# Kernel optimization log

Hardware: AMD Instinct MI355X
Metric: run time of the kernel (lower is better)

The kernel has to match this reference:

```python
import jax, jax.numpy as jnp
import numpy as np

EPS = 1e-8  # torch cosine_similarity norm clamp

def _cos(a, b, axis=-1):
    na = jnp.maximum(jnp.linalg.norm(a, axis=axis), EPS)
    nb = jnp.maximum(jnp.linalg.norm(b, axis=axis), EPS)
    return jnp.sum(a * b, axis=axis) / (na * nb)

def setup_inputs() -> dict:
    key = jax.random.key(0)
    ks = jax.random.split(key, 9)
    B, L, D, S = 8, 8192, 512, 131072
    scale = 0.02
    x = jax.random.normal(ks[0], (B, L, D), jnp.float32)
    context_W = jax.random.normal(ks[1], (D, D), jnp.float32) * scale
    context_b = jnp.zeros((D,), jnp.float32)
    pred_W1 = jax.random.normal(ks[2], (D, D), jnp.float32) * scale
    pred_b1 = jnp.zeros((D,), jnp.float32)
    pred_W2 = jax.random.normal(ks[3], (D, D), jnp.float32) * scale
    pred_b2 = jnp.zeros((D,), jnp.float32)
    raw_embeddings = jax.random.normal(ks[4], (S, D), jnp.float32)
    u = jax.random.uniform(ks[5], (S,), jnp.float32)
    surprise_level = jnp.where(u > 0.5, u, 0.0)  # ~half the slots active
    return {"x": x, "context_W": context_W, "context_b": context_b,
            "pred_W1": pred_W1, "pred_b1": pred_b1,
            "pred_W2": pred_W2, "pred_b2": pred_b2,
            "raw_embeddings": raw_embeddings, "surprise_level": surprise_level}

def reference(x, context_W, context_b, pred_W1, pred_b1, pred_W2, pred_b2,
              raw_embeddings, surprise_level):
    # context = pad(x[:, :-1], left-shift by one along seq), i.e. causal previous token
    context = jnp.pad(x[:, :-1, :], ((0, 0), (1, 0), (0, 0)))
    # predictor MLP on projected context (torch Linear: y = x @ W.T + b)
    ctx = context @ context_W.T + context_b
    h = jax.nn.gelu(ctx @ pred_W1.T + pred_b1, approximate=False)
    prediction = h @ pred_W2.T + pred_b2  # [B, L, D]
    mse = jnp.mean((x - prediction) ** 2, axis=-1)
    prediction_surprise = jnp.sqrt(mse)  # [B, L]

    # memory-contrastive surprise: cosine sim of pooled x vs active stored embeddings
    active = surprise_level > 0  # [S]
    x_pooled = jnp.mean(x, axis=1)  # [B, D]
    sim = _cos(x_pooled[:, None, :], raw_embeddings[None, :, :])  # [B, S]
    sim = jnp.where(active[None, :], sim, -jnp.inf)
    max_sim = jnp.max(sim, axis=-1)           # [B]
    best_idx = jnp.argmax(sim, axis=-1)       # [B]
    best_stored = raw_embeddings[best_idx]    # [B, D] argmax-based gather
    divergence = 1.0 - _cos(x, best_stored[:, None, :])  # [B, L]
    pattern_match = (max_sim[:, None] > 0.3).astype(x.dtype)
    contrastive = pattern_match * divergence

    surprise = jnp.maximum(prediction_surprise, contrastive * 2.0)  # [B, L]
    return surprise
```

## Files before the change

### kernel.cpp

```cpp
#include <hip/hip_runtime.h>
#include <math.h>

#define OFF_SIMKEY   0
#define OFF_POOLED   1024
#define ZEROED_BYTES 17408
#define OFF_MAXSIM   17408
#define OFF_NORME    17664
#define OFF_EBEST    17920
#define OFF_BPRIME   34304
#define OFF_WP       36864
#define OFF_W2B      561152

typedef __attribute__((ext_vector_type(8))) short bf16x8;
typedef __attribute__((ext_vector_type(4))) float f32x4;

__device__ inline unsigned short f2bf(float f) {
    unsigned int u = __float_as_uint(f);
    unsigned int r = (u + 0x7FFFu + ((u >> 16) & 1u)) >> 16;
    return (unsigned short)r;
}

__device__ inline void load_lds_16(const void* g, void* l) {
    __builtin_amdgcn_global_load_lds((const __attribute__((address_space(1))) void*)g,
                                     (__attribute__((address_space(3))) void*)l, 16, 0, 0);
}

__global__ void __launch_bounds__(256) k_pre(const float* __restrict__ W1, const float* __restrict__ Wc,
                      const float* __restrict__ b1, const float* __restrict__ bc,
                      unsigned short* __restrict__ Wp, float* __restrict__ bprime) {
    __shared__ float w1row[512];
    __shared__ float wsum[4];
    int t = threadIdx.x;
    int n = blockIdx.x >> 1, half = blockIdx.x & 1;
    if (t < 128) ((float4*)w1row)[t] = ((const float4*)(W1 + (size_t)n * 512))[t];
    __syncthreads();
    int k = half * 256 + t;
    float acc = 0.f;
#pragma unroll 8
    for (int j = 0; j < 512; ++j) acc += w1row[j] * Wc[(size_t)j * 512 + k];
    Wp[(size_t)n * 512 + k] = f2bf(acc);
    if (half == 0) {
        float p = w1row[t] * bc[t] + w1row[t + 256] * bc[t + 256];
#pragma unroll
        for (int m = 32; m >= 1; m >>= 1) p += __shfl_xor(p, m);
        if ((t & 63) == 0) wsum[t >> 6] = p;
        __syncthreads();
        if (t == 0) bprime[n] = b1[n] + wsum[0] + wsum[1] + wsum[2] + wsum[3];
    }
}

__global__ void __launch_bounds__(256) k_cast(const float* __restrict__ W2, unsigned short* __restrict__ W2b) {
    int i = blockIdx.x * 1024 + threadIdx.x * 4;
    float4 v = *(const float4*)(W2 + i);
    ushort4 o;
    o.x = f2bf(v.x); o.y = f2bf(v.y); o.z = f2bf(v.z); o.w = f2bf(v.w);
    *(ushort4*)(W2b + i) = o;
}

__global__ void __launch_bounds__(512) k_pool(const float* __restrict__ x, float* __restrict__ pooled) {
    __shared__ float4 pb[4][128];
    int t = threadIdx.x;
    int q = t & 127;
    int rg = t >> 7;
    int b = blockIdx.y;
    int l0 = blockIdx.x * 128;
    const float4* p = (const float4*)(x + ((size_t)b * 8192 + l0 + rg) * 512) + q;
    float4 s = make_float4(0.f, 0.f, 0.f, 0.f);
#pragma unroll 8
    for (int i = 0; i < 32; ++i) {
        float4 v = p[(size_t)i * 512];
        s.x += v.x; s.y += v.y; s.z += v.z; s.w += v.w;
    }
    pb[rg][q] = s;
    __syncthreads();
    if (rg == 0) {
        float4 a = pb[0][q], b1_ = pb[1][q], c = pb[2][q], d = pb[3][q];
        atomicAdd(&pooled[b * 512 + q * 4 + 0], a.x + b1_.x + c.x + d.x);
        atomicAdd(&pooled[b * 512 + q * 4 + 1], a.y + b1_.y + c.y + d.y);
        atomicAdd(&pooled[b * 512 + q * 4 + 2], a.z + b1_.z + c.z + d.z);
        atomicAdd(&pooled[b * 512 + q * 4 + 3], a.w + b1_.w + c.w + d.w);
    }
}

__global__ void __launch_bounds__(256) k_sim(const float* __restrict__ E, const float* __restrict__ sl,
                     const float* __restrict__ pooledws, unsigned long long* __restrict__ simkey) {
    __shared__ float ps[4096];
    __shared__ unsigned long long wkey[4][8];
    int t = threadIdx.x, lane = t & 63, w = t >> 6;
#pragma unroll
    for (int c = 0; c < 16; ++c) ps[t + c * 256] = pooledws[t + c * 256] * (1.0f / 8192.0f);
    __syncthreads();
    float pr[8][8];
#pragma unroll
    for (int b = 0; b < 8; ++b) {
        float4 v0 = *(const float4*)&ps[b * 512 + lane * 8];
        float4 v1 = *(const float4*)&ps[b * 512 + lane * 8 + 4];
        pr[b][0] = v0.x; pr[b][1] = v0.y; pr[b][2] = v0.z; pr[b][3] = v0.w;
        pr[b][4] = v1.x; pr[b][5] = v1.y; pr[b][6] = v1.z; pr[b][7] = v1.w;
    }
    float npinv[8];
#pragma unroll
    for (int b = 0; b < 8; ++b) {
        float s = 0.f;
#pragma unroll
        for (int j = 0; j < 8; ++j) s += pr[b][j] * pr[b][j];
#pragma unroll
        for (int m = 32; m >= 1; m >>= 1) s += __shfl_xor(s, m);
        npinv[b] = 1.0f / fmaxf(sqrtf(s), 1e-8f);
    }
    unsigned long long best[8];
#pragma unroll
    for (int b = 0; b < 8; ++b) best[b] = 0ull;
    int sbase = blockIdx.x * 64 + w * 16;
    float mysl = (lane < 16) ? sl[sbase + lane] : 0.f;
    unsigned long long mask = __ballot(mysl > 0.0f);
    for (int it = 0; it < 16; ++it) {
        if (!((mask >> it) & 1ull)) continue;
        int s = sbase + it;
        const float4* ep = (const float4*)(E + (size_t)s * 512);
        float4 e0 = ep[lane * 2], e1 = ep[lane * 2 + 1];
        float nrm = e0.x * e0.x + e0.y * e0.y + e0.z * e0.z + e0.w * e0.w
                  + e1.x * e1.x + e1.y * e1.y + e1.z * e1.z + e1.w * e1.w;
        float dt[8];
#pragma unroll
        for (int b = 0; b < 8; ++b)
            dt[b] = e0.x * pr[b][0] + e0.y * pr[b][1] + e0.z * pr[b][2] + e0.w * pr[b][3]
                  + e1.x * pr[b][4] + e1.y * pr[b][5] + e1.z * pr[b][6] + e1.w * pr[b][7];
#pragma unroll
        for (int m = 32; m >= 1; m >>= 1) {
            nrm += __shfl_xor(nrm, m);
#pragma unroll
            for (int b = 0; b < 8; ++b) dt[b] += __shfl_xor(dt[b], m);
        }
        float neinv = 1.0f / fmaxf(sqrtf(nrm), 1e-8f);
#pragma unroll
        for (int b = 0; b < 8; ++b) {
            float sim = dt[b] * npinv[b] * neinv;
            unsigned int u = __float_as_uint(sim);
            unsigned int k32 = (u & 0x80000000u) ? ~u : (u | 0x80000000u);
            unsigned long long key = ((unsigned long long)k32 << 32) | (unsigned int)(~(unsigned int)s);
            if (key > best[b]) best[b] = key;
        }
    }
    if (lane == 0) {
#pragma unroll
        for (int b = 0; b < 8; ++b) wkey[w][b] = best[b];
    }
    __syncthreads();
    if (t < 8) {
        unsigned long long k = wkey[0][t];
#pragma unroll
        for (int w2 = 1; w2 < 4; ++w2) if (wkey[w2][t] > k) k = wkey[w2][t];
        if (k) atomicMax(&simkey[t], k);
    }
}

__global__ void __launch_bounds__(64) k_b2(const float* __restrict__ E, const unsigned long long* __restrict__ simkey,
                    float* __restrict__ max_sim, float* __restrict__ norm_e, float* __restrict__ ebest) {
    int b = blockIdx.x, lane = threadIdx.x;
    unsigned long long key = simkey[b];
    float ms; unsigned int idx;
    if (key == 0ull) { ms = -1e30f; idx = 0u; }
    else {
        unsigned int k32 = (unsigned int)(key >> 32);
        unsigned int u = (k32 & 0x80000000u) ? (k32 & 0x7FFFFFFFu) : ~k32;
        ms = __uint_as_float(u);
        idx = ~(unsigned int)(key & 0xFFFFFFFFull);
    }
    const float4* ep = (const float4*)(E + (size_t)idx * 512);
    float4 e0 = ep[lane * 2], e1 = ep[lane * 2 + 1];
    *(float4*)&ebest[b * 512 + lane * 8] = e0;
    *(float4*)&ebest[b * 512 + lane * 8 + 4] = e1;
    float s = e0.x * e0.x + e0.y * e0.y + e0.z * e0.z + e0.w * e0.w
            + e1.x * e1.x + e1.y * e1.y + e1.z * e1.z + e1.w * e1.w;
#pragma unroll
    for (int m = 32; m >= 1; m >>= 1) s += __shfl_xor(s, m);
    if (lane == 0) { max_sim[b] = ms; norm_e[b] = fmaxf(sqrtf(s), 1e-8f); }
}

__global__ void __launch_bounds__(1024, 4) k_mega(
        const float* __restrict__ x, const unsigned short* __restrict__ Wp,
        const float* __restrict__ bprime, const unsigned short* __restrict__ W2b,
        const float* __restrict__ b2, const float* __restrict__ ebest,
        const float* __restrict__ max_sim, const float* __restrict__ norm_e,
        float* __restrict__ out) {
    __shared__ char smem[114688];
    unsigned short* Hs = (unsigned short*)(smem);
    unsigned short* Bs = (unsigned short*)(smem + 65536);
    unsigned short* Ts = (unsigned short*)(smem + 98304);
    unsigned int*  Ts32 = (unsigned int*)Ts;
    float* red = (float*)(smem + 102400);

    const int t = threadIdx.x;
    const int lane = t & 63, w = t >> 6;
    const int l15 = lane & 15, quad = lane >> 4;
    const int r = t >> 4, cp = t & 15;
    const int gr0 = blockIdx.x * 64;
    const int b = gr0 >> 13;

    unsigned int areg[16];
    {
        int gr = gr0 + r;
        bool z = ((gr & 8191) == 0);
        const float* src = x + ((size_t)gr - 1) * 512 + cp * 2;
#pragma unroll
        for (int k = 0; k < 16; ++k) {
            float2 v = make_float2(0.f, 0.f);
            if (!z) v = *(const float2*)(src + k * 32);
            areg[k] = (unsigned int)f2bf(v.x) | ((unsigned int)f2bf(v.y) << 16);
        }
    }

    f32x4 acc[4][2];
#pragma unroll
    for (int i = 0; i < 4; ++i)
#pragma unroll
        for (int j = 0; j < 2; ++j) acc[i][j] = (f32x4){0.f, 0.f, 0.f, 0.f};
#pragma unroll
    for (int kt = 0; kt < 16; ++kt) {
        __syncthreads();
        Ts32[r * 16 + cp] = areg[kt];
#pragma unroll
        for (int c = 0; c < 2; ++c) {
            int unit = c * 1024 + t;
            load_lds_16(Wp + (size_t)(unit >> 2) * 512 + kt * 32 + (unit & 3) * 8,
                        Bs + c * 8192 + w * 512);
        }
        __syncthreads();
        bf16x8 af[4], bfr[2];
#pragma unroll
        for (int i = 0; i < 4; ++i)
            af[i] = *(const bf16x8*)&Ts[(i * 16 + l15) * 32 + quad * 8];
#pragma unroll
        for (int j = 0; j < 2; ++j)
            bfr[j] = *(const bf16x8*)&Bs[(w * 32 + j * 16 + l15) * 32 + quad * 8];
#pragma unroll
        for (int i = 0; i < 4; ++i)
#pragma unroll
            for (int j = 0; j < 2; ++j)
                acc[i][j] = __builtin_amdgcn_mfma_f32_16x16x32_bf16(af[i], bfr[j], acc[i][j], 0, 0, 0);
    }
    {
        float bpj[2];
#pragma unroll
        for (int j = 0; j < 2; ++j) bpj[j] = bprime[w * 32 + j * 16 + l15];
#pragma unroll
        for (int i = 0; i < 4; ++i)
#pragma unroll
            for (int j = 0; j < 2; ++j)
#pragma unroll
                for (int rg = 0; rg < 4; ++rg) {
                    int m = i * 16 + quad * 4 + rg;
                    int n = w * 32 + j * 16 + l15;
                    float v = acc[i][j][rg] + bpj[j];
                    v = 0.5f * v * (1.0f + erff(v * 0.70710678118f));
                    Hs[(n >> 5) * 2048 + m * 32 + (n & 31)] = f2bf(v);
                }
    }

    f32x4 acc2[4][2];
#pragma unroll
    for (int i = 0; i < 4; ++i)
#pragma unroll
        for (int j = 0; j < 2; ++j) acc2[i][j] = (f32x4){0.f, 0.f, 0.f, 0.f};
#pragma unroll
    for (int kt = 0; kt < 16; ++kt) {
        __syncthreads();
#pragma unroll
        for (int c = 0; c < 2; ++c) {
            int unit = c * 1024 + t;
            load_lds_16(W2b + (size_t)(unit >> 2) * 512 + kt * 32 + (unit & 3) * 8,
                        Bs + c * 8192 + w * 512);
        }
        __syncthreads();
        bf16x8 af[4], bfr[2];
#pragma unroll
        for (int i = 0; i < 4; ++i)
            af[i] = *(const bf16x8*)&Hs[kt * 2048 + (i * 16 + l15) * 32 + quad * 8];
#pragma unroll
        for (int j = 0; j < 2; ++j)
            bfr[j] = *(const bf16x8*)&Bs[(w * 32 + j * 16 + l15) * 32 + quad * 8];
#pragma unroll
        for (int i = 0; i < 4; ++i)
#pragma unroll
            for (int j = 0; j < 2; ++j)
                acc2[i][j] = __builtin_amdgcn_mfma_f32_16x16x32_bf16(af[i], bfr[j], acc2[i][j], 0, 0, 0);
    }

    {
        float b2j[2], ej[2];
#pragma unroll
        for (int j = 0; j < 2; ++j) {
            int n = w * 32 + j * 16 + l15;
            b2j[j] = b2[n];
            ej[j] = ebest[b * 512 + n];
        }
#pragma unroll
        for (int i = 0; i < 4; ++i)
#pragma unroll
            for (int rg = 0; rg < 4; ++rg) {
                int m = i * 16 + quad * 4 + rg;
                int gr = gr0 + m;
                float sd = 0.f, sx = 0.f, sdt = 0.f;
#pragma unroll
                for (int j = 0; j < 2; ++j) {
                    int n = w * 32 + j * 16 + l15;
                    float p = acc2[i][j][rg] + b2j[j];
                    float xv = x[(size_t)gr * 512 + n];
                    float d = xv - p;
                    sd += d * d; sx += xv * xv; sdt += xv * ej[j];
                }
#pragma unroll
                for (int mm = 8; mm >= 1; mm >>= 1) {
                    sd += __shfl_xor(sd, mm);
                    sx += __shfl_xor(sx, mm);
                    sdt += __shfl_xor(sdt, mm);
                }
                if (l15 == 0) {
                    red[(m * 16 + w) * 3 + 0] = sd;
                    red[(m * 16 + w) * 3 + 1] = sx;
                    red[(m * 16 + w) * 3 + 2] = sdt;
                }
            }
    }
    __syncthreads();
    if (t < 64) {
        float sd = 0.f, sx = 0.f, sdt = 0.f;
#pragma unroll
        for (int w2 = 0; w2 < 16; ++w2) {
            sd  += red[(t * 16 + w2) * 3 + 0];
            sx  += red[(t * 16 + w2) * 3 + 1];
            sdt += red[(t * 16 + w2) * 3 + 2];
        }
        float ps = sqrtf(sd * (1.0f / 512.0f));
        float ms = max_sim[b];
        float c = 0.f;
        if (ms > 0.3f) {
            float nx = fmaxf(sqrtf(sx), 1e-8f);
            c = 2.0f * (1.0f - sdt / (nx * norm_e[b]));
        }
        out[gr0 + t] = fmaxf(ps, c);
    }
}

extern "C" void kernel_launch(void* const* d_in, const int* in_sizes, int n_in,
                              void* d_out, int out_size, void* d_ws, size_t ws_size,
                              hipStream_t stream) {
    const float* x  = (const float*)d_in[0];
    const float* Wc = (const float*)d_in[1];
    const float* bc = (const float*)d_in[2];
    const float* W1 = (const float*)d_in[3];
    const float* b1 = (const float*)d_in[4];
    const float* W2 = (const float*)d_in[5];
    const float* b2 = (const float*)d_in[6];
    const float* E  = (const float*)d_in[7];
    const float* sl = (const float*)d_in[8];

    char* ws = (char*)d_ws;
    unsigned long long* simkey = (unsigned long long*)(ws + OFF_SIMKEY);
    float* pooled  = (float*)(ws + OFF_POOLED);
    float* max_sim = (float*)(ws + OFF_MAXSIM);
    float* norm_e  = (float*)(ws + OFF_NORME);
    float* ebest   = (float*)(ws + OFF_EBEST);
    float* bprime  = (float*)(ws + OFF_BPRIME);
    unsigned short* Wp  = (unsigned short*)(ws + OFF_WP);
    unsigned short* W2b = (unsigned short*)(ws + OFF_W2B);
    float* out = (float*)d_out;

    hipMemsetAsync(ws, 0, ZEROED_BYTES, stream);
    k_pre<<<1024, 256, 0, stream>>>(W1, Wc, b1, bc, Wp, bprime);
    k_cast<<<256, 256, 0, stream>>>(W2, W2b);
    k_pool<<<dim3(64, 8), 512, 0, stream>>>(x, pooled);
    k_sim<<<2048, 256, 0, stream>>>(E, sl, pooled, simkey);
    k_b2<<<8, 64, 0, stream>>>(E, simkey, max_sim, norm_e, ebest);
    k_mega<<<1024, 1024, 0, stream>>>(x, Wp, bprime, W2b, b2, ebest, max_sim, norm_e, out);
}
```

Measured before the change: 705.3 us.

## Double-buffer LDS tiles, swizzle layouts, and halve block size in fused MLP kernel

The fused MLP kernel now runs 512 threads per block, with each wave computing a 64x64 tile (4x4 MFMAs) instead of 32 columns. Weight and activation K-tiles are double-buffered in LDS, so the next tile's loads are issued before the current MFMAs and each iteration needs one barrier instead of two. The first W2 tile is prefetched during the last GEMM1 step. XOR swizzling is applied to the Ts, Bs and Hs layouts to avoid LDS bank conflicts. In exchange, LDS use grows to about 142KB per block, which limits residency to one block per CU, and the larger accumulator tile raises register pressure.

```diff
diff --git a/kernel.cpp b/kernel.cpp
--- a/kernel.cpp
+++ b/kernel.cpp
@@ -178,120 +178,151 @@
     if (lane == 0) { max_sim[b] = ms; norm_e[b] = fmaxf(sqrtf(s), 1e-8f); }
 }
 
-__global__ void __launch_bounds__(1024, 4) k_mega(
+__global__ void __launch_bounds__(512, 2) k_mega(
         const float* __restrict__ x, const unsigned short* __restrict__ Wp,
         const float* __restrict__ bprime, const unsigned short* __restrict__ W2b,
         const float* __restrict__ b2, const float* __restrict__ ebest,
         const float* __restrict__ max_sim, const float* __restrict__ norm_e,
         float* __restrict__ out) {
-    __shared__ char smem[114688];
+    __shared__ char smem[145408];
     unsigned short* Hs = (unsigned short*)(smem);
     unsigned short* Bs = (unsigned short*)(smem + 65536);
-    unsigned short* Ts = (unsigned short*)(smem + 98304);
-    unsigned int*  Ts32 = (unsigned int*)Ts;
-    float* red = (float*)(smem + 102400);
+    unsigned int*  Ts32 = (unsigned int*)(smem + 131072);
+    unsigned short* Ts = (unsigned short*)(smem + 131072);
+    float* red = (float*)(smem + 139264);
 
     const int t = threadIdx.x;
     const int lane = t & 63, w = t >> 6;
     const int l15 = lane & 15, quad = lane >> 4;
-    const int r = t >> 4, cp = t & 15;
     const int gr0 = blockIdx.x * 64;
     const int b = gr0 >> 13;
 
-    unsigned int areg[16];
+    int srcB[4];
+#pragma unroll
+    for (int c = 0; c < 4; ++c) {
+        int off16 = c * 512 + t;
+        int row = off16 >> 2, slot = off16 & 3;
+        int g = slot ^ ((row >> 1) & 3);
+        srcB[c] = row * 512 + g * 8;
+    }
+    const int r = t >> 3, cc = t & 7;
+    const int sR = (r >> 1) & 3;
+    const int d0 = (((cc >> 2) ^ sR) << 2) | (cc & 3);
+    const int d1 = ((((cc >> 2) + 2) ^ sR) << 2) | (cc & 3);
+    int tsoff[4], bsoff[4], hoff[4];
+#pragma unroll
+    for (int i = 0; i < 4; ++i) {
+        int rowA = i * 16 + l15;
+        tsoff[i] = rowA * 32 + ((quad ^ ((rowA >> 1) & 3)) << 3);
+        hoff[i]  = rowA * 32 + ((quad ^ ((rowA >> 2) & 3)) << 3);
+        int rowB = w * 64 + i * 16 + l15;
+        bsoff[i] = rowB * 32 + ((quad ^ ((rowB >> 1) & 3)) << 3);
+    }
+
+    unsigned int alo[16], ahi[16];
     {
         int gr = gr0 + r;
         bool z = ((gr & 8191) == 0);
-        const float* src = x + ((size_t)gr - 1) * 512 + cp * 2;
-#pragma unroll
-        for (int k = 0; k < 16; ++k) {
-            float2 v = make_float2(0.f, 0.f);
-            if (!z) v = *(const float2*)(src + k * 32);
-            areg[k] = (unsigned int)f2bf(v.x) | ((unsigned int)f2bf(v.y) << 16);
-        }
-    }
-
-    f32x4 acc[4][2];
+        const float* src = x + ((size_t)gr - 1) * 512 + cc * 2;
+#pragma unroll
+        for (int kt = 0; kt < 16; ++kt) {
+            float2 v0 = make_float2(0.f, 0.f), v1 = make_float2(0.f, 0.f);
+            if (!z) { v0 = *(const float2*)(src + kt * 32); v1 = *(const float2*)(src + kt * 32 + 16); }
+            alo[kt] = (unsigned int)f2bf(v0.x) | ((unsigned int)f2bf(v0.y) << 16);
+            ahi[kt] = (unsigned int)f2bf(v1.x) | ((unsigned int)f2bf(v1.y) << 16);
+        }
+    }
+
+    Ts32[r * 16 + d0] = alo[0];
+    Ts32[r * 16 + d1] = ahi[0];
+#pragma unroll
+    for (int c = 0; c < 4; ++c)
+        load_lds_16(Wp + srcB[c], Bs + c * 4096 + w * 512);
+    __syncthreads();
+
+    f32x4 acc[4][4];
 #pragma unroll
     for (int i = 0; i < 4; ++i)
 #pragma unroll
-        for (int j = 0; j < 2; ++j) acc[i][j] = (f32x4){0.f, 0.f, 0.f, 0.f};
+        for (int j = 0; j < 4; ++j) acc[i][j] = (f32x4){0.f, 0.f, 0.f, 0.f};
 #pragma unroll
     for (int kt = 0; kt < 16; ++kt) {
+        const int cur = kt & 1, nxt = cur ^ 1;
+        if (kt < 15) {
+            Ts32[nxt * 1024 + r * 16 + d0] = alo[kt + 1];
+            Ts32[nxt * 1024 + r * 16 + d1] = ahi[kt + 1];
+#pragma unroll
+            for (int c = 0; c < 4; ++c)
+                load_lds_16(Wp + srcB[c] + (kt + 1) * 32, Bs + nxt * 16384 + c * 4096 + w * 512);
+        } else {
+#pragma unroll
+            for (int c = 0; c < 4; ++c)
+                load_lds_16(W2b + srcB[c], Bs + c * 4096 + w * 512);
+        }
+        bf16x8 af[4], bfr[4];
+#pragma unroll
+        for (int i = 0; i < 4; ++i) af[i] = *(const bf16x8*)&Ts[cur * 2048 + tsoff[i]];
+#pragma unroll
+        for (int j = 0; j < 4; ++j) bfr[j] = *(const bf16x8*)&Bs[cur * 16384 + bsoff[j]];
+#pragma unroll
+        for (int i = 0; i < 4; ++i)
+#pragma unroll
+            for (int j = 0; j < 4; ++j)
+                acc[i][j] = __builtin_amdgcn_mfma_f32_16x16x32_bf16(af[i], bfr[j], acc[i][j], 0, 0, 0);
         __syncthreads();
-        Ts32[r * 16 + cp] = areg[kt];
-#pragma unroll
-        for (int c = 0; c < 2; ++c) {
-            int unit = c * 1024 + t;
-            load_lds_16(Wp + (size_t)(unit >> 2) * 512 + kt * 32 + (unit & 3) * 8,
-                        Bs + c * 8192 + w * 512);
-        }
-        __syncthreads();
-        bf16x8 af[4], bfr[2];
+    }
+
+    {
+        float bpj[4];
+#pragma unroll
+        for (int j = 0; j < 4; ++j) bpj[j] = bprime[w * 64 + j * 16 + l15];
 #pragma unroll
         for (int i = 0; i < 4; ++i)
-            af[i] = *(const bf16x8*)&Ts[(i * 16 + l15) * 32 + quad * 8];
-#pragma unroll
-        for (int j = 0; j < 2; ++j)
-            bfr[j] = *(const bf16x8*)&Bs[(w * 32 + j * 16 + l15) * 32 + quad * 8];
-#pragma unroll
-        for (int i = 0; i < 4; ++i)
-#pragma unroll
-            for (int j = 0; j < 2; ++j)
-                acc[i][j] = __builtin_amdgcn_mfma_f32_16x16x32_bf16(af[i], bfr[j], acc[i][j], 0, 0, 0);
-    }
-    {
-        float bpj[2];
-#pragma unroll
-        for (int j = 0; j < 2; ++j) bpj[j] = bprime[w * 32 + j * 16 + l15];
-#pragma unroll
-        for (int i = 0; i < 4; ++i)
-#pragma unroll
-            for (int j = 0; j < 2; ++j)
+#pragma unroll
+            for (int j = 0; j < 4; ++j)
 #pragma unroll
                 for (int rg = 0; rg < 4; ++rg) {
                     int m = i * 16 + quad * 4 + rg;
-                    int n = w * 32 + j * 16 + l15;
+                    int ktc = w * 2 + (j >> 1);
+                    int grp = ((j & 1) * 2 + (l15 >> 3)) ^ ((m >> 2) & 3);
                     float v = acc[i][j][rg] + bpj[j];
                     v = 0.5f * v * (1.0f + erff(v * 0.70710678118f));
-                    Hs[(n >> 5) * 2048 + m * 32 + (n & 31)] = f2bf(v);
+                    Hs[ktc * 2048 + m * 32 + grp * 8 + (l15 & 7)] = f2bf(v);
                 }
     }
-
-    f32x4 acc2[4][2];
+    __syncthreads();
+
+    f32x4 acc2[4][4];
 #pragma unroll
     for (int i = 0; i < 4; ++i)
 #pragma unroll
-        for (int j = 0; j < 2; ++j) acc2[i][j] = (f32x4){0.f, 0.f, 0.f, 0.f};
+        for (int j = 0; j < 4; ++j) acc2[i][j] = (f32x4){0.f, 0.f, 0.f, 0.f};
 #pragma unroll
     for (int kt = 0; kt < 16; ++kt) {
-        __syncthreads();
-#pragma unroll
-        for (int c = 0; c < 2; ++c) {
-            int unit = c * 1024 + t;
-            load_lds_16(W2b + (size_t)(unit >> 2) * 512 + kt * 32 + (unit & 3) * 8,
-                        Bs + c * 8192 + w * 512);
-        }
-        __syncthreads();
-        bf16x8 af[4], bfr[2];
+        const int cur = kt & 1, nxt = cur ^ 1;
+        if (kt < 15) {
+#pragma unroll
+            for (int c = 0; c < 4; ++c)
+                load_lds_16(W2b + srcB[c] + (kt + 1) * 32, Bs + nxt * 16384 + c * 4096 + w * 512);
+        }
+        bf16x8 af[4], bfr[4];
+#pragma unroll
+        for (int i = 0; i < 4; ++i) af[i] = *(const bf16x8*)&Hs[kt * 2048 + hoff[i]];
+#pragma unroll
+        for (int j = 0; j < 4; ++j) bfr[j] = *(const bf16x8*)&Bs[cur * 16384 + bsoff[j]];
 #pragma unroll
         for (int i = 0; i < 4; ++i)
-            af[i] = *(const bf16x8*)&Hs[kt * 2048 + (i * 16 + l15) * 32 + quad * 8];
-#pragma unroll
-        for (int j = 0; j < 2; ++j)
-            bfr[j] = *(const bf16x8*)&Bs[(w * 32 + j * 16 + l15) * 32 + quad * 8];
-#pragma unroll
-        for (int i = 0; i < 4; ++i)
-#pragma unroll
-            for (int j = 0; j < 2; ++j)
+#pragma unroll
+            for (int j = 0; j < 4; ++j)
                 acc2[i][j] = __builtin_amdgcn_mfma_f32_16x16x32_bf16(af[i], bfr[j], acc2[i][j], 0, 0, 0);
+        if (kt < 15) __syncthreads();
     }
 
     {
-        float b2j[2], ej[2];
-#pragma unroll
-        for (int j = 0; j < 2; ++j) {
-            int n = w * 32 + j * 16 + l15;
+        float b2j[4], ej[4];
+#pragma unroll
+        for (int j = 0; j < 4; ++j) {
+            int n = w * 64 + j * 16 + l15;
             b2j[j] = b2[n];
             ej[j] = ebest[b * 512 + n];
         }
@@ -303,8 +334,8 @@
                 int gr = gr0 + m;
                 float sd = 0.f, sx = 0.f, sdt = 0.f;
 #pragma unroll
-                for (int j = 0; j < 2; ++j) {
-                    int n = w * 32 + j * 16 + l15;
+                for (int j = 0; j < 4; ++j) {
+                    int n = w * 64 + j * 16 + l15;
                     float p = acc2[i][j][rg] + b2j[j];
                     float xv = x[(size_t)gr * 512 + n];
                     float d = xv - p;
@@ -317,9 +348,9 @@
                     sdt += __shfl_xor(sdt, mm);
                 }
                 if (l15 == 0) {
-                    red[(m * 16 + w) * 3 + 0] = sd;
-                    red[(m * 16 + w) * 3 + 1] = sx;
-                    red[(m * 16 + w) * 3 + 2] = sdt;
+                    red[(m * 8 + w) * 3 + 0] = sd;
+                    red[(m * 8 + w) * 3 + 1] = sx;
+                    red[(m * 8 + w) * 3 + 2] = sdt;
                 }
             }
     }
@@ -327,10 +358,10 @@
     if (t < 64) {
         float sd = 0.f, sx = 0.f, sdt = 0.f;
 #pragma unroll
-        for (int w2 = 0; w2 < 16; ++w2) {
-            sd  += red[(t * 16 + w2) * 3 + 0];
-            sx  += red[(t * 16 + w2) * 3 + 1];
-            sdt += red[(t * 16 + w2) * 3 + 2];
+        for (int w2 = 0; w2 < 8; ++w2) {
+            sd  += red[(t * 8 + w2) * 3 + 0];
+            sx  += red[(t * 8 + w2) * 3 + 1];
+            sdt += red[(t * 8 + w2) * 3 + 2];
         }
         float ps = sqrtf(sd * (1.0f / 512.0f));
         float ms = max_sim[b];
@@ -373,5 +404,5 @@
     k_pool<<<dim3(64, 8), 512, 0, stream>>>(x, pooled);
     k_sim<<<2048, 256, 0, stream>>>(E, sl, pooled, simkey);
     k_b2<<<8, 64, 0, stream>>>(E, simkey, max_sim, norm_e, ebest);
-    k_mega<<<1024, 1024, 0, stream>>>(x, Wp, bprime, W2b, b2, ebest, max_sim, norm_e, out);
-}
+    k_mega<<<1024, 512, 0, stream>>>(x, Wp, bprime, W2b, b2, ebest, max_sim, norm_e, out);
+}
```

New measurement: 657.6 us. 6.8% less time.
